# Kernel tuning notes

Measured on AMD Instinct MI355X. Metric: run time of the kernel, lower is better.

The kernel has to match this reference:

```python
import jax, jax.numpy as jnp
import numpy as np

T, B, L = 4, 8192, 50
VOCAB, D = 100000, 128


def setup_inputs() -> dict:
    key = jax.random.key(0)
    ks = jax.random.split(key, 10)
    inp = {
        "indices": jax.random.randint(ks[0], (T, B, L), 0, VOCAB, dtype=jnp.int32),
        "lengths": jax.random.randint(ks[1], (T, B), 0, L, dtype=jnp.int32),
        "tables": jax.random.normal(ks[2], (T, VOCAB, D), dtype=jnp.float32) * 0.02,
        "W1": jax.random.normal(ks[3], (D, D), dtype=jnp.float32) * (1.0 / np.sqrt(D)),
        "b1": jax.random.normal(ks[4], (D,), dtype=jnp.float32) * 0.01,
        "W2": jax.random.normal(ks[5], (D, D), dtype=jnp.float32) * (1.0 / np.sqrt(D)),
        "b2": jax.random.normal(ks[6], (D,), dtype=jnp.float32) * 0.01,
        "W3": jax.random.normal(ks[7], (D, D), dtype=jnp.float32) * (1.0 / np.sqrt(D)),
        "b3": jax.random.normal(ks[8], (D,), dtype=jnp.float32) * 0.01,
    }
    return inp


def reference(indices, lengths, tables, W1, b1, W2, b2, W3, b3):
    # Per-table jagged gather + SUM pooling (EmbeddingBagCollection default).
    t, b, l = indices.shape
    emb = jax.vmap(lambda tab, idx: tab[idx])(tables, indices)  # [T,B,L,D]
    mask = (jnp.arange(l, dtype=lengths.dtype) < lengths[..., None])[..., None]
    pooled = jnp.sum(jnp.where(mask, emb, jnp.zeros((), emb.dtype)), axis=2)  # [T,B,D]
    # torch.cat over dict values concatenates along dim 0 -> [T*B, D]
    x = pooled.reshape(t * b, -1)
    # nn.Sequential of three Linear(D, D) layers, no activation
    x = x @ W1.T + b1
    x = x @ W2.T + b2
    x = x @ W3.T + b3
    return x
```

## Files before the change

kernel.cpp:

```cpp
#include <hip/hip_runtime.h>


#define T_ 4
#define B_ 8192
#define L_ 50
#define VOCAB_ 100000
#define D_ 128
#define ROWS 16
#define NBAGS (T_ * B_)

#define WS_M  0
#define WS_C  16384

__global__ __launch_bounds__(128) void combine(const float* __restrict__ W1,
                                               const float* __restrict__ W2,
                                               const float* __restrict__ W3,
                                               const float* __restrict__ b1,
                                               const float* __restrict__ b2,
                                               const float* __restrict__ b3,
                                               float* __restrict__ ws) {
  __shared__ float a1[D_];
  const int j = threadIdx.x;
  const int i = blockIdx.x;
  if (i < D_) {
    float acc = 0.f;
    for (int k = 0; k < D_; ++k)
      acc += W1[k * D_ + i] * W2[j * D_ + k];
    a1[j] = acc;
    __syncthreads();
    float m = 0.f;
    for (int k = 0; k < D_; ++k)
      m += a1[k] * W3[j * D_ + k];
    ws[WS_M + i * D_ + j] = m;
  } else {
    float c1 = b2[j];
    for (int k = 0; k < D_; ++k)
      c1 += b1[k] * W2[j * D_ + k];
    a1[j] = c1;
    __syncthreads();
    float c = b3[j];
    for (int k = 0; k < D_; ++k)
      c += a1[k] * W3[j * D_ + k];
    ws[WS_C + j] = c;
  }
}

__global__ __launch_bounds__(256, 8) void fused(const int* __restrict__ indices,
                                                const int* __restrict__ lengths,
                                                const float* __restrict__ tables,
                                                const float* __restrict__ ws,
                                                float* __restrict__ out) {
  __shared__ __align__(16) float pooled_sh[ROWS][D_];
  __shared__ int off_sh[ROWS][L_];
  __shared__ int len_sh[ROWS];
  __shared__ int bag_ctr;

  const int tid = threadIdx.x;
  const int g0  = blockIdx.x * ROWS;

  if (tid == 0) bag_ctr = 0;
  for (int k = tid; k < ROWS * L_; k += 256)
    off_sh[k / L_][k % L_] = indices[g0 * L_ + k] << 9;
  if (tid < ROWS) len_sh[tid] = lengths[g0 + tid];
  __syncthreads();

  {
    const int lane = tid & 63;
    const int half = lane >> 5;
    const int d0   = (lane & 31) * 4;
    const int t    = g0 >> 13;
    const char* __restrict__ tab =
        (const char*)(tables + (size_t)t * (VOCAB_ * D_) + d0);

    for (;;) {
      int pos = 0;
      if (lane == 0) pos = atomicAdd(&bag_ctr, 1);
      pos = __shfl(pos, 0, 64);
      if (pos >= ROWS) break;
      const int len = len_sh[pos];
      const int* __restrict__ il = off_sh[pos];
      float ax = 0.f, ay = 0.f, az = 0.f, aw = 0.f;
      int l = 0;
      for (; l + 7 < len; l += 8) {
        const int o0 = il[l + 0 + half];
        const int o1 = il[l + 2 + half];
        const int o2 = il[l + 4 + half];
        const int o3 = il[l + 6 + half];
        const float4 v0 = *(const float4*)(tab + o0);
        const float4 v1 = *(const float4*)(tab + o1);
        const float4 v2 = *(const float4*)(tab + o2);
        const float4 v3 = *(const float4*)(tab + o3);
        ax += v0.x; ay += v0.y; az += v0.z; aw += v0.w;
        ax += v1.x; ay += v1.y; az += v1.z; aw += v1.w;
        ax += v2.x; ay += v2.y; az += v2.z; aw += v2.w;
        ax += v3.x; ay += v3.y; az += v3.z; aw += v3.w;
      }
      for (; l + 1 < len; l += 2) {
        const float4 v = *(const float4*)(tab + il[l + half]);
        ax += v.x; ay += v.y; az += v.z; aw += v.w;
      }
      if (l < len && half == 0) {
        const float4 v = *(const float4*)(tab + il[l]);
        ax += v.x; ay += v.y; az += v.z; aw += v.w;
      }
      ax += __shfl_xor(ax, 32, 64);
      ay += __shfl_xor(ay, 32, 64);
      az += __shfl_xor(az, 32, 64);
      aw += __shfl_xor(aw, 32, 64);
      if (half == 0)
        *(float4*)&pooled_sh[pos][d0] = make_float4(ax, ay, az, aw);
    }
  }
  __syncthreads();

  const int jc = (tid & 63) * 2;
  const int rh = (tid >> 6) * 4;
  const float* __restrict__ Mg = ws + WS_M;
  const float2 c2 = *(const float2*)(ws + WS_C + jc);
  float2 a0 = c2, a1 = c2, a2 = c2, a3 = c2;
#pragma unroll 4
  for (int i = 0; i < D_; ++i) {
    const float2 m = *(const float2*)(Mg + i * D_ + jc);
    const float p0 = pooled_sh[rh + 0][i];
    const float p1 = pooled_sh[rh + 1][i];
    const float p2 = pooled_sh[rh + 2][i];
    const float p3 = pooled_sh[rh + 3][i];
    a0.x += p0 * m.x; a0.y += p0 * m.y;
    a1.x += p1 * m.x; a1.y += p1 * m.y;
    a2.x += p2 * m.x; a2.y += p2 * m.y;
    a3.x += p3 * m.x; a3.y += p3 * m.y;
  }
  *(float2*)&out[(size_t)(g0 + rh + 0) * D_ + jc] = a0;
  *(float2*)&out[(size_t)(g0 + rh + 1) * D_ + jc] = a1;
  *(float2*)&out[(size_t)(g0 + rh + 2) * D_ + jc] = a2;
  *(float2*)&out[(size_t)(g0 + rh + 3) * D_ + jc] = a3;
}

extern "C" void kernel_launch(void* const* d_in, const int* in_sizes, int n_in,
                              void* d_out, int out_size, void* d_ws, size_t ws_size,
                              hipStream_t stream) {
  const int*   indices = (const int*)d_in[0];
  const int*   lengths = (const int*)d_in[1];
  const float* tables  = (const float*)d_in[2];
  const float* W1      = (const float*)d_in[3];
  const float* b1      = (const float*)d_in[4];
  const float* W2      = (const float*)d_in[5];
  const float* b2      = (const float*)d_in[6];
  const float* W3      = (const float*)d_in[7];
  const float* b3      = (const float*)d_in[8];
  float*       out     = (float*)d_out;
  float*       ws      = (float*)d_ws;

  combine<<<D_ + 1, D_, 0, stream>>>(W1, W2, W3, b1, b2, b3, ws);
  fused<<<NBAGS / ROWS, 256, 0, stream>>>(indices, lengths, tables, ws, out);
}
```

Measured before the change: 348.8 us.

## Switch to persistent kernel with global atomic bag queue per wavefront

Replaces the one-block-per-16-bags grid with 1024 persistent blocks. Each wavefront pulls individual bags from a global atomic counter in the workspace, which combine() resets. Each wave pools four bags into private shared memory, then applies the combined matrix and writes them out, so there are no block-wide barriers and uneven bag lengths are balanced dynamically. The gather loop is also unrolled to 16 entries per iteration. In exchange it pays one global atomic per bag, loads indices and lengths per bag with no prefetch, and relies on wave-level ordering of shared-memory accesses.

```diff
diff --git a/kernel.cpp b/kernel.cpp
--- a/kernel.cpp
+++ b/kernel.cpp
@@ -6,11 +6,11 @@
 #define L_ 50
 #define VOCAB_ 100000
 #define D_ 128
-#define ROWS 16
 #define NBAGS (T_ * B_)
 
-#define WS_M  0
-#define WS_C  16384
+#define WS_M   0
+#define WS_C   16384
+#define WS_CTR 16512
 
 __global__ __launch_bounds__(128) void combine(const float* __restrict__ W1,
                                                const float* __restrict__ W2,
@@ -33,6 +33,7 @@
       m += a1[k] * W3[j * D_ + k];
     ws[WS_M + i * D_ + j] = m;
   } else {
+    if (j == 0) ((int*)ws)[WS_CTR] = 0;
     float c1 = b2[j];
     for (int k = 0; k < D_; ++k)
       c1 += b1[k] * W2[j * D_ + k];
@@ -45,95 +46,167 @@
   }
 }
 
-__global__ __launch_bounds__(256, 8) void fused(const int* __restrict__ indices,
+__global__ __launch_bounds__(256, 4) void fused(const int* __restrict__ indices,
                                                 const int* __restrict__ lengths,
                                                 const float* __restrict__ tables,
-                                                const float* __restrict__ ws,
+                                                float* __restrict__ ws,
                                                 float* __restrict__ out) {
-  __shared__ __align__(16) float pooled_sh[ROWS][D_];
-  __shared__ int off_sh[ROWS][L_];
-  __shared__ int len_sh[ROWS];
-  __shared__ int bag_ctr;
-
-  const int tid = threadIdx.x;
-  const int g0  = blockIdx.x * ROWS;
-
-  if (tid == 0) bag_ctr = 0;
-  for (int k = tid; k < ROWS * L_; k += 256)
-    off_sh[k / L_][k % L_] = indices[g0 * L_ + k] << 9;
-  if (tid < ROWS) len_sh[tid] = lengths[g0 + tid];
-  __syncthreads();
-
-  {
-    const int lane = tid & 63;
-    const int half = lane >> 5;
-    const int d0   = (lane & 31) * 4;
-    const int t    = g0 >> 13;
+  __shared__ __align__(16) float p_sh[4][4][D_];
+  __shared__ int off_sh[4][64];
+
+  const int wid  = threadIdx.x >> 6;
+  const int lane = threadIdx.x & 63;
+  const int half = lane >> 5;
+  const int d0   = (lane & 31) * 4;
+  const int jc   = lane * 2;
+
+  int* __restrict__ ctr = (int*)ws + WS_CTR;
+  const float* __restrict__ Mg = ws + WS_M;
+  const float2 c2 = *(const float2*)(ws + WS_C + jc);
+
+  float* __restrict__ pw = &p_sh[wid][0][0];
+  int*   __restrict__ ow = off_sh[wid];
+
+  int id0 = -1, id1 = -1, id2 = -1, id3 = -1;
+  int s = 0;
+
+  for (;;) {
+    int b = 0;
+    if (lane == 0) b = atomicAdd(ctr, 1);
+    b = __shfl(b, 0, 64);
+    if (b >= NBAGS) break;
+
+    const int len = lengths[b];
+    if (lane < L_) ow[lane] = indices[b * L_ + lane] << 9;
+    asm volatile("s_waitcnt lgkmcnt(0)" ::: "memory");
+
+    const int t = b >> 13;
     const char* __restrict__ tab =
         (const char*)(tables + (size_t)t * (VOCAB_ * D_) + d0);
 
-    for (;;) {
-      int pos = 0;
-      if (lane == 0) pos = atomicAdd(&bag_ctr, 1);
-      pos = __shfl(pos, 0, 64);
-      if (pos >= ROWS) break;
-      const int len = len_sh[pos];
-      const int* __restrict__ il = off_sh[pos];
-      float ax = 0.f, ay = 0.f, az = 0.f, aw = 0.f;
-      int l = 0;
-      for (; l + 7 < len; l += 8) {
-        const int o0 = il[l + 0 + half];
-        const int o1 = il[l + 2 + half];
-        const int o2 = il[l + 4 + half];
-        const int o3 = il[l + 6 + half];
-        const float4 v0 = *(const float4*)(tab + o0);
-        const float4 v1 = *(const float4*)(tab + o1);
-        const float4 v2 = *(const float4*)(tab + o2);
-        const float4 v3 = *(const float4*)(tab + o3);
-        ax += v0.x; ay += v0.y; az += v0.z; aw += v0.w;
-        ax += v1.x; ay += v1.y; az += v1.z; aw += v1.w;
-        ax += v2.x; ay += v2.y; az += v2.z; aw += v2.w;
-        ax += v3.x; ay += v3.y; az += v3.z; aw += v3.w;
+    float ax = 0.f, ay = 0.f, az = 0.f, aw = 0.f;
+    int l = 0;
+    for (; l + 15 < len; l += 16) {
+      const int o0 = ow[l +  0 + half];
+      const int o1 = ow[l +  2 + half];
+      const int o2 = ow[l +  4 + half];
+      const int o3 = ow[l +  6 + half];
+      const int o4 = ow[l +  8 + half];
+      const int o5 = ow[l + 10 + half];
+      const int o6 = ow[l + 12 + half];
+      const int o7 = ow[l + 14 + half];
+      const float4 v0 = *(const float4*)(tab + o0);
+      const float4 v1 = *(const float4*)(tab + o1);
+      const float4 v2 = *(const float4*)(tab + o2);
+      const float4 v3 = *(const float4*)(tab + o3);
+      const float4 v4 = *(const float4*)(tab + o4);
+      const float4 v5 = *(const float4*)(tab + o5);
+      const float4 v6 = *(const float4*)(tab + o6);
+      const float4 v7 = *(const float4*)(tab + o7);
+      ax += v0.x; ay += v0.y; az += v0.z; aw += v0.w;
+      ax += v1.x; ay += v1.y; az += v1.z; aw += v1.w;
+      ax += v2.x; ay += v2.y; az += v2.z; aw += v2.w;
+      ax += v3.x; ay += v3.y; az += v3.z; aw += v3.w;
+      ax += v4.x; ay += v4.y; az += v4.z; aw += v4.w;
+      ax += v5.x; ay += v5.y; az += v5.z; aw += v5.w;
+      ax += v6.x; ay += v6.y; az += v6.z; aw += v6.w;
+      ax += v7.x; ay += v7.y; az += v7.z; aw += v7.w;
+    }
+    if (l + 7 < len) {
+      const int o0 = ow[l + 0 + half];
+      const int o1 = ow[l + 2 + half];
+      const int o2 = ow[l + 4 + half];
+      const int o3 = ow[l + 6 + half];
+      const float4 v0 = *(const float4*)(tab + o0);
+      const float4 v1 = *(const float4*)(tab + o1);
+      const float4 v2 = *(const float4*)(tab + o2);
+      const float4 v3 = *(const float4*)(tab + o3);
+      ax += v0.x; ay += v0.y; az += v0.z; aw += v0.w;
+      ax += v1.x; ay += v1.y; az += v1.z; aw += v1.w;
+      ax += v2.x; ay += v2.y; az += v2.z; aw += v2.w;
+      ax += v3.x; ay += v3.y; az += v3.z; aw += v3.w;
+      l += 8;
+    }
+    if (l + 3 < len) {
+      const int o0 = ow[l + 0 + half];
+      const int o1 = ow[l + 2 + half];
+      const float4 v0 = *(const float4*)(tab + o0);
+      const float4 v1 = *(const float4*)(tab + o1);
+      ax += v0.x; ay += v0.y; az += v0.z; aw += v0.w;
+      ax += v1.x; ay += v1.y; az += v1.z; aw += v1.w;
+      l += 4;
+    }
+    if (l + 1 < len) {
+      const float4 v = *(const float4*)(tab + ow[l + half]);
+      ax += v.x; ay += v.y; az += v.z; aw += v.w;
+      l += 2;
+    }
+    if (l < len && half == 0) {
+      const float4 v = *(const float4*)(tab + ow[l]);
+      ax += v.x; ay += v.y; az += v.z; aw += v.w;
+    }
+    ax += __shfl_xor(ax, 32, 64);
+    ay += __shfl_xor(ay, 32, 64);
+    az += __shfl_xor(az, 32, 64);
+    aw += __shfl_xor(aw, 32, 64);
+    if (half == 0)
+      *(float4*)(pw + s * D_ + d0) = make_float4(ax, ay, az, aw);
+
+    if (s == 0) id0 = b; else if (s == 1) id1 = b;
+    else if (s == 2) id2 = b; else id3 = b;
+    ++s;
+
+    if (s == 4) {
+      asm volatile("s_waitcnt lgkmcnt(0)" ::: "memory");
+      float2 a0 = c2, a1 = c2, a2 = c2, a3 = c2;
+#pragma unroll 4
+      for (int i = 0; i < D_; ++i) {
+        const float2 m = *(const float2*)(Mg + i * D_ + jc);
+        const float q0 = pw[0 * D_ + i];
+        const float q1 = pw[1 * D_ + i];
+        const float q2 = pw[2 * D_ + i];
+        const float q3 = pw[3 * D_ + i];
+        a0.x += q0 * m.x; a0.y += q0 * m.y;
+        a1.x += q1 * m.x; a1.y += q1 * m.y;
+        a2.x += q2 * m.x; a2.y += q2 * m.y;
+        a3.x += q3 * m.x; a3.y += q3 * m.y;
       }
-      for (; l + 1 < len; l += 2) {
-        const float4 v = *(const float4*)(tab + il[l + half]);
-        ax += v.x; ay += v.y; az += v.z; aw += v.w;
-      }
-      if (l < len && half == 0) {
-        const float4 v = *(const float4*)(tab + il[l]);
-        ax += v.x; ay += v.y; az += v.z; aw += v.w;
-      }
-      ax += __shfl_xor(ax, 32, 64);
-      ay += __shfl_xor(ay, 32, 64);
-      az += __shfl_xor(az, 32, 64);
-      aw += __shfl_xor(aw, 32, 64);
-      if (half == 0)
-        *(float4*)&pooled_sh[pos][d0] = make_float4(ax, ay, az, aw);
-    }
-  }
-  __syncthreads();
-
-  const int jc = (tid & 63) * 2;
-  const int rh = (tid >> 6) * 4;
-  const float* __restrict__ Mg = ws + WS_M;
-  const float2 c2 = *(const float2*)(ws + WS_C + jc);
-  float2 a0 = c2, a1 = c2, a2 = c2, a3 = c2;
-#pragma unroll 4
-  for (int i = 0; i < D_; ++i) {
-    const float2 m = *(const float2*)(Mg + i * D_ + jc);
-    const float p0 = pooled_sh[rh + 0][i];
-    const float p1 = pooled_sh[rh + 1][i];
-    const float p2 = pooled_sh[rh + 2][i];
-    const float p3 = pooled_sh[rh + 3][i];
-    a0.x += p0 * m.x; a0.y += p0 * m.y;
-    a1.x += p1 * m.x; a1.y += p1 * m.y;
-    a2.x += p2 * m.x; a2.y += p2 * m.y;
-    a3.x += p3 * m.x; a3.y += p3 * m.y;
-  }
-  *(float2*)&out[(size_t)(g0 + rh + 0) * D_ + jc] = a0;
-  *(float2*)&out[(size_t)(g0 + rh + 1) * D_ + jc] = a1;
-  *(float2*)&out[(size_t)(g0 + rh + 2) * D_ + jc] = a2;
-  *(float2*)&out[(size_t)(g0 + rh + 3) * D_ + jc] = a3;
+      *(float2*)&out[(size_t)id0 * D_ + jc] = a0;
+      *(float2*)&out[(size_t)id1 * D_ + jc] = a1;
+      *(float2*)&out[(size_t)id2 * D_ + jc] = a2;
+      *(float2*)&out[(size_t)id3 * D_ + jc] = a3;
+      s = 0;
+    }
+  }
+
+  asm volatile("s_waitcnt lgkmcnt(0)" ::: "memory");
+  if (s > 0) {
+    float2 a0 = c2;
+#pragma unroll 4
+    for (int i = 0; i < D_; ++i) {
+      const float2 m = *(const float2*)(Mg + i * D_ + jc);
+      a0.x += pw[0 * D_ + i] * m.x; a0.y += pw[0 * D_ + i] * m.y;
+    }
+    *(float2*)&out[(size_t)id0 * D_ + jc] = a0;
+  }
+  if (s > 1) {
+    float2 a0 = c2;
+#pragma unroll 4
+    for (int i = 0; i < D_; ++i) {
+      const float2 m = *(const float2*)(Mg + i * D_ + jc);
+      a0.x += pw[1 * D_ + i] * m.x; a0.y += pw[1 * D_ + i] * m.y;
+    }
+    *(float2*)&out[(size_t)id1 * D_ + jc] = a0;
+  }
+  if (s > 2) {
+    float2 a0 = c2;
+#pragma unroll 4
+    for (int i = 0; i < D_; ++i) {
+      const float2 m = *(const float2*)(Mg + i * D_ + jc);
+      a0.x += pw[2 * D_ + i] * m.x; a0.y += pw[2 * D_ + i] * m.y;
+    }
+    *(float2*)&out[(size_t)id2 * D_ + jc] = a0;
+  }
 }
 
 extern "C" void kernel_launch(void* const* d_in, const int* in_sizes, int n_in,
@@ -152,5 +225,5 @@
   float*       ws      = (float*)d_ws;
 
   combine<<<D_ + 1, D_, 0, stream>>>(W1, W2, W3, b1, b2, b3, ws);
-  fused<<<NBAGS / ROWS, 256, 0, stream>>>(indices, lengths, tables, ws, out);
+  fused<<<1024, 256, 0, stream>>>(indices, lengths, tables, ws, out);
 }
```

New measurement: 681.8 us. 95.4% more time.
